# Optimization experiments

Measured on AMD Instinct MI355X. Metric: run time of the kernel, lower is better.

Reference implementation:

```python
import jax, jax.numpy as jnp
import numpy as np

V, D, L, H, T = 32000, 1024, 4, 16, 1024
DH = D // H
SCALE = DH ** -0.5
FF = 4 * D
R = 2  # n_rounds


def setup_inputs() -> dict:
    key = jax.random.key(0)
    ks = iter(jax.random.split(key, 32))
    s = 0.02
    nrm = lambda shape: jax.random.normal(next(ks), shape, dtype=jnp.float32) * s
    inp = {
        "x": jax.random.randint(next(ks), (2, T), 0, V),
        "embed": nrm((V, D)),
        "pos_embed": nrm((T, D)),
        "Wqkv": nrm((L, R, 3 * D, D)),
        "bqkv": jnp.zeros((L, R, 3 * D), jnp.float32),
        "Wo": nrm((L, D, D)),
        "bo": jnp.zeros((L, D), jnp.float32),
        "Wg": nrm((L, D, 2 * D)),
        "bg": jnp.zeros((L, D), jnp.float32),
        "ln1_g": jnp.ones((L, D), jnp.float32),
        "ln1_b": jnp.zeros((L, D), jnp.float32),
        "W1": nrm((L, FF, D)),
        "b1": jnp.zeros((L, FF), jnp.float32),
        "W2": nrm((L, D, FF)),
        "b2": jnp.zeros((L, D), jnp.float32),
        "ln2_g": jnp.ones((L, D), jnp.float32),
        "ln2_b": jnp.zeros((L, D), jnp.float32),
        "lnf_g": jnp.ones((D,), jnp.float32),
        "lnf_b": jnp.zeros((D,), jnp.float32),
    }
    return inp


def _ln(h, g, b, eps=1e-5):
    m = jnp.mean(h, axis=-1, keepdims=True)
    v = jnp.mean((h - m) ** 2, axis=-1, keepdims=True)
    return (h - m) * jax.lax.rsqrt(v + eps) * g + b


def _attend(h, W, b, mask):
    B, Tq, _ = h.shape
    qkv = (h @ W.T + b).reshape(B, Tq, 3, H, DH)
    q, k, v = qkv[:, :, 0], qkv[:, :, 1], qkv[:, :, 2]  # [B,T,H,DH]
    scores = jnp.einsum("bqhd,bkhd->bhqk", q, k) * SCALE
    scores = jnp.where(mask, scores, -jnp.inf)
    a = jax.nn.softmax(scores, axis=-1)
    return jnp.einsum("bhqk,bkhd->bqhd", a, v).reshape(B, Tq, D)


def reference(x, embed, pos_embed, Wqkv, bqkv, Wo, bo, Wg, bg,
              ln1_g, ln1_b, W1, b1, W2, b2, ln2_g, ln2_b, lnf_g, lnf_b):
    B, Tq = x.shape
    mask = jnp.tril(jnp.ones((Tq, Tq), dtype=bool))
    h = embed[x] + pos_embed[jnp.arange(Tq)]
    for l in range(L):
        n1 = _ln(h, ln1_g[l], ln1_b[l])
        pred = _attend(n1, Wqkv[l, 0], bqkv[l, 0], mask)
        cum = pred
        out = pred
        # boosted round 2: attend on residual, gate the correction
        corr = _attend(n1 - cum, Wqkv[l, 1], bqkv[l, 1], mask)
        gate = jax.nn.sigmoid(jnp.concatenate([cum, corr], axis=-1) @ Wg[l].T + bg[l])
        gated = gate * corr
        out = out + gated
        h = h + (out @ Wo[l].T + bo[l])
        n2 = _ln(h, ln2_g[l], ln2_b[l])
        ff = jax.nn.gelu(n2 @ W1[l].T + b1[l], approximate=False) @ W2[l].T + b2[l]
        h = h + ff
    return _ln(h, lnf_g, lnf_b) @ embed.T  # tied head, no bias
```

## Files before the change

kernel.cpp:

```cpp
#include <hip/hip_runtime.h>
#include <math.h>

#define D_  1024
#define T_  1024
#define B_  2
#define H_  16
#define DH_ 64
#define L_  4
#define FF_ 4096
#define V_  32000
#define M_  2048

typedef _Float16 f16;
typedef _Float16 f16x8 __attribute__((ext_vector_type(8)));
typedef _Float16 f16x4 __attribute__((ext_vector_type(4)));
typedef float    fx4  __attribute__((ext_vector_type(4)));

__global__ __launch_bounds__(256) void f2h_k(const float* __restrict__ in, f16* __restrict__ out) {
    const long i = ((long)blockIdx.x * 256 + threadIdx.x) * 4;
    const float4 v = *(const float4*)(in + i);
    f16x4 o = { (f16)v.x, (f16)v.y, (f16)v.z, (f16)v.w };
    *(f16x4*)(out + i) = o;
}

__global__ __launch_bounds__(256) void embed_k(const int* __restrict__ x, const float* __restrict__ emb,
                                               const float* __restrict__ pos, float* __restrict__ h) {
    const long m = blockIdx.x;
    const int  t = threadIdx.x;
    const long tok = x[m];
    const long pt  = m & (T_ - 1);
    const float4 e = ((const float4*)(emb + tok * D_))[t];
    const float4 p = ((const float4*)(pos + pt * D_))[t];
    ((float4*)(h + m * D_))[t] = make_float4(e.x + p.x, e.y + p.y, e.z + p.z, e.w + p.w);
}

__global__ __launch_bounds__(256) void ln_k(const float* __restrict__ x, const float* __restrict__ g,
                                            const float* __restrict__ b, float* __restrict__ of,
                                            f16* __restrict__ oh) {
    const long m = blockIdx.x;
    const int  t = threadIdx.x;
    const int  wave = t >> 6, lane = t & 63;
    __shared__ float red1[4], red2[4];
    const float4 v = ((const float4*)(x + m * D_))[t];
    float s = v.x + v.y + v.z + v.w;
#pragma unroll
    for (int off = 32; off; off >>= 1) s += __shfl_xor(s, off, 64);
    if (lane == 0) red1[wave] = s;
    __syncthreads();
    const float mean = (red1[0] + red1[1] + red1[2] + red1[3]) * (1.0f / 1024.0f);
    const float d0 = v.x - mean, d1 = v.y - mean, d2 = v.z - mean, d3 = v.w - mean;
    float s2 = d0 * d0 + d1 * d1 + d2 * d2 + d3 * d3;
#pragma unroll
    for (int off = 32; off; off >>= 1) s2 += __shfl_xor(s2, off, 64);
    if (lane == 0) red2[wave] = s2;
    __syncthreads();
    const float var  = (red2[0] + red2[1] + red2[2] + red2[3]) * (1.0f / 1024.0f);
    const float rstd = rsqrtf(var + 1e-5f);
    const float4 gv = ((const float4*)g)[t];
    const float4 bv = ((const float4*)b)[t];
    const float o0 = d0 * rstd * gv.x + bv.x;
    const float o1 = d1 * rstd * gv.y + bv.y;
    const float o2 = d2 * rstd * gv.z + bv.z;
    const float o3 = d3 * rstd * gv.w + bv.w;
    if (of) ((float4*)(of + m * D_))[t] = make_float4(o0, o1, o2, o3);
    if (oh) { f16x4 o = { (f16)o0, (f16)o1, (f16)o2, (f16)o3 }; *(f16x4*)(oh + m * D_ + t * 4) = o; }
}

__global__ __launch_bounds__(256) void sub_k(const float* __restrict__ a, const float* __restrict__ b,
                                             f16* __restrict__ o) {
    const long i = ((long)blockIdx.x * 256 + threadIdx.x) * 4;
    const float4 va = *(const float4*)(a + i);
    const float4 vb = *(const float4*)(b + i);
    f16x4 o4 = { (f16)(va.x - vb.x), (f16)(va.y - vb.y), (f16)(va.z - vb.z), (f16)(va.w - vb.w) };
    *(f16x4*)(o + i) = o4;
}

__global__ __launch_bounds__(256) void cat_k(const float* __restrict__ p, const float* __restrict__ c,
                                             f16* __restrict__ o) {
    const long i = ((long)blockIdx.x * 256 + threadIdx.x) * 4;
    const long m = i >> 11;
    const int  j = (int)(i & 2047);
    const float* src = (j < 1024) ? (p + m * 1024 + j) : (c + m * 1024 + (j - 1024));
    const float4 v = *(const float4*)src;
    f16x4 o4 = { (f16)v.x, (f16)v.y, (f16)v.z, (f16)v.w };
    *(f16x4*)(o + i) = o4;
}

__global__ __launch_bounds__(256) void gate_k(const float* __restrict__ p, const float* __restrict__ c,
                                              const float* __restrict__ gl, f16* __restrict__ o) {
    const long i = ((long)blockIdx.x * 256 + threadIdx.x) * 4;
    const float4 vp = *(const float4*)(p + i);
    const float4 vc = *(const float4*)(c + i);
    const float4 vg = *(const float4*)(gl + i);
    const float s0 = 1.0f / (1.0f + __expf(-vg.x));
    const float s1 = 1.0f / (1.0f + __expf(-vg.y));
    const float s2 = 1.0f / (1.0f + __expf(-vg.z));
    const float s3 = 1.0f / (1.0f + __expf(-vg.w));
    f16x4 o4 = { (f16)(vp.x + s0 * vc.x), (f16)(vp.y + s1 * vc.y),
                 (f16)(vp.z + s2 * vc.z), (f16)(vp.w + s3 * vc.w) };
    *(f16x4*)(o + i) = o4;
}

template<int BN>
__global__ __launch_bounds__(256)
void gemm_bt(const f16* __restrict__ A, const f16* __restrict__ Wt,
             const float* __restrict__ bias, const float* __restrict__ resid,
             float* __restrict__ Cf, f16* __restrict__ Ch,
             int N, int K, int gelu) {
    __shared__ __align__(16) f16 As[128 * 32];
    __shared__ __align__(16) f16 Bs[BN * 32];
    const int tid  = threadIdx.x;
    const int wave = tid >> 6;
    const int lane = tid & 63;

    const int nbm = gridDim.y;
    const int nbn = gridDim.x;
    int bi = blockIdx.y * nbn + blockIdx.x;
    const int nwg = nbm * nbn;
    if ((nwg & 7) == 0) bi = (bi & 7) * (nwg >> 3) + (bi >> 3);
    const long bm = bi % nbm;
    const long bn = bi / nbm;

    const int wm = (wave >> 1) * 64;
    const int wn = (wave & 1) * (BN / 2);
    constexpr int NJ = BN / 32;

    fx4 acc[4][NJ] = {};

    const int c0 = wave * 2;
    const int r0 = c0 * 16 + (lane >> 2);
    const int cc = (lane & 3) * 8;
    const f16* a0 = A + ((long)bm * 128 + r0) * K + cc;
    const f16* a1 = A + ((long)bm * 128 + r0 + 16) * K + cc;
    f16* sa0 = &As[c0 * 512];
    f16* sa1 = &As[(c0 + 1) * 512];

    const f16* b0;
    const f16* b1 = nullptr;
    f16* sb0;
    f16* sb1 = nullptr;
    if constexpr (BN == 128) {
        b0  = Wt + ((long)bn * 128 + r0) * K + cc;
        b1  = Wt + ((long)bn * 128 + r0 + 16) * K + cc;
        sb0 = &Bs[c0 * 512];
        sb1 = &Bs[(c0 + 1) * 512];
    } else {
        b0  = Wt + ((long)bn * 64 + wave * 16 + (lane >> 2)) * K + cc;
        sb0 = &Bs[wave * 512];
    }

    for (int k0 = 0; k0 < K; k0 += 32) {
        __builtin_amdgcn_global_load_lds((const __attribute__((address_space(1))) void*)(a0 + k0),
                                         (__attribute__((address_space(3))) void*)sa0, 16, 0, 0);
        __builtin_amdgcn_global_load_lds((const __attribute__((address_space(1))) void*)(a1 + k0),
                                         (__attribute__((address_space(3))) void*)sa1, 16, 0, 0);
        __builtin_amdgcn_global_load_lds((const __attribute__((address_space(1))) void*)(b0 + k0),
                                         (__attribute__((address_space(3))) void*)sb0, 16, 0, 0);
        if constexpr (BN == 128)
            __builtin_amdgcn_global_load_lds((const __attribute__((address_space(1))) void*)(b1 + k0),
                                             (__attribute__((address_space(3))) void*)sb1, 16, 0, 0);
        __syncthreads();
        const int koff = (lane >> 4) * 8;
        f16x8 af[4], bf[NJ];
#pragma unroll
        for (int i = 0; i < 4; ++i)
            af[i] = *(const f16x8*)&As[(wm + i * 16 + (lane & 15)) * 32 + koff];
#pragma unroll
        for (int j = 0; j < NJ; ++j)
            bf[j] = *(const f16x8*)&Bs[(wn + j * 16 + (lane & 15)) * 32 + koff];
#pragma unroll
        for (int i = 0; i < 4; ++i)
#pragma unroll
            for (int j = 0; j < NJ; ++j)
                acc[i][j] = __builtin_amdgcn_mfma_f32_16x16x32_f16(af[i], bf[j], acc[i][j], 0, 0, 0);
        __syncthreads();
    }

    const long gr_base = bm * 128 + wm + (lane >> 4) * 4;
    const long gc_base = bn * BN + wn + (lane & 15);
#pragma unroll
    for (int i = 0; i < 4; ++i) {
#pragma unroll
        for (int j = 0; j < NJ; ++j) {
            const long gc = gc_base + j * 16;
            const float bv = bias ? bias[gc] : 0.0f;
#pragma unroll
            for (int r = 0; r < 4; ++r) {
                const long gr = gr_base + i * 16 + r;
                float v = acc[i][j][r] + bv;
                if (gelu) v = 0.5f * v * (1.0f + erff(v * 0.70710678118654752f));
                else if (resid) v += resid[gr * (long)N + gc];
                if (Cf) Cf[gr * (long)N + gc] = v;
                if (Ch) Ch[gr * (long)N + gc] = (f16)v;
            }
        }
    }
}

__global__ __launch_bounds__(256) void fattn_k(const f16* __restrict__ qkv, float* __restrict__ out) {
    __shared__ __align__(16) f16 Ks[64 * 72];
    __shared__ __align__(16) f16 Vt[64 * 72];
    __shared__ __align__(16) f16 Pw[4][16 * 72];
    const int tid  = threadIdx.x;
    const int w    = tid >> 6;
    const int lane = tid & 63;
    const int b  = blockIdx.z, h = blockIdx.y;
    const int qt = (gridDim.x - 1) - blockIdx.x;
    const int q0w = qt * 64 + w * 16;
    const int g  = lane >> 4;
    const int lm = lane & 15;

    const long qrow = ((long)(b * T_ + q0w + lm)) * (3 * D_) + h * DH_;
    f16x8 af_q[2];
    af_q[0] = *(const f16x8*)(qkv + qrow + g * 8);
    af_q[1] = *(const f16x8*)(qkv + qrow + 32 + g * 8);

    float m_r[4], l_r[4];
    fx4 acc_o[4] = {};
#pragma unroll
    for (int r = 0; r < 4; ++r) { m_r[r] = -INFINITY; l_r[r] = 0.0f; }

    const int srow = tid >> 2;
    const int scol = (tid & 3) * 16;
    const long kbase = ((long)(b * T_)) * (3 * D_) + D_ + h * DH_ + scol;
    const long vbase = kbase + D_;

    const int nkb = qt + 1;
    for (int it = 0; it < nkb; ++it) {
        const int kb = it * 64;
        __syncthreads();
        {
            const f16* ksrc = qkv + kbase + (long)(kb + srow) * (3 * D_);
            f16x8 k0 = *(const f16x8*)(ksrc);
            f16x8 k1 = *(const f16x8*)(ksrc + 8);
            *(f16x8*)&Ks[srow * 72 + scol]     = k0;
            *(f16x8*)&Ks[srow * 72 + scol + 8] = k1;
            const f16* vsrc = qkv + vbase + (long)(kb + srow) * (3 * D_);
            f16x8 v0 = *(const f16x8*)(vsrc);
            f16x8 v1 = *(const f16x8*)(vsrc + 8);
#pragma unroll
            for (int i = 0; i < 8; ++i) {
                const int d = scol + i;
                Vt[d * 72 + (srow ^ (((d >> 2) & 7) << 3))] = v0[i];
            }
#pragma unroll
            for (int i = 0; i < 8; ++i) {
                const int d = scol + 8 + i;
                Vt[d * 72 + (srow ^ (((d >> 2) & 7) << 3))] = v1[i];
            }
        }
        __syncthreads();

        fx4 sc[4];
#pragma unroll
        for (int kt = 0; kt < 4; ++kt) {
            fx4 c = {};
#pragma unroll
            for (int kk = 0; kk < 2; ++kk) {
                f16x8 bf = *(const f16x8*)&Ks[(kt * 16 + lm) * 72 + kk * 32 + g * 8];
                c = __builtin_amdgcn_mfma_f32_16x16x32_f16(af_q[kk], bf, c, 0, 0, 0);
            }
            sc[kt] = c * 0.125f;
        }
        if (kb == qt * 64) {
#pragma unroll
            for (int kt = 0; kt < 4; ++kt) {
                const int key_g = kb + kt * 16 + lm;
#pragma unroll
                for (int r = 0; r < 4; ++r)
                    if (key_g > q0w + g * 4 + r) sc[kt][r] = -INFINITY;
            }
        }

        float mnew[4], pscale[4];
#pragma unroll
        for (int r = 0; r < 4; ++r) {
            float tm = fmaxf(fmaxf(sc[0][r], sc[1][r]), fmaxf(sc[2][r], sc[3][r]));
#pragma unroll
            for (int off = 8; off; off >>= 1) tm = fmaxf(tm, __shfl_xor(tm, off, 64));
            mnew[r]   = fmaxf(m_r[r], tm);
            pscale[r] = __expf(m_r[r] - mnew[r]);
        }
        float psum[4] = {};
#pragma unroll
        for (int kt = 0; kt < 4; ++kt) {
#pragma unroll
            for (int r = 0; r < 4; ++r) {
                const float p = __expf(sc[kt][r] - mnew[r]);
                sc[kt][r] = p;
                psum[r] += p;
            }
        }
#pragma unroll
        for (int r = 0; r < 4; ++r) {
#pragma unroll
            for (int off = 8; off; off >>= 1) psum[r] += __shfl_xor(psum[r], off, 64);
            l_r[r] = l_r[r] * pscale[r] + psum[r];
            m_r[r] = mnew[r];
        }
#pragma unroll
        for (int nt = 0; nt < 4; ++nt)
#pragma unroll
            for (int r = 0; r < 4; ++r) acc_o[nt][r] *= pscale[r];

        f16* P = Pw[w];
#pragma unroll
        for (int kt = 0; kt < 4; ++kt)
#pragma unroll
            for (int r = 0; r < 4; ++r)
                P[(g * 4 + r) * 72 + kt * 16 + lm] = (f16)sc[kt][r];

#pragma unroll
        for (int kc = 0; kc < 2; ++kc) {
            f16x8 ap = *(const f16x8*)&P[lm * 72 + kc * 32 + g * 8];
#pragma unroll
            for (int nt = 0; nt < 4; ++nt) {
                const int d = nt * 16 + lm;
                const int col = (kc * 32 + g * 8) ^ (((d >> 2) & 7) << 3);
                f16x8 bv = *(const f16x8*)&Vt[d * 72 + col];
                acc_o[nt] = __builtin_amdgcn_mfma_f32_16x16x32_f16(ap, bv, acc_o[nt], 0, 0, 0);
            }
        }
    }

    const long obase = ((long)(b * T_ + q0w + g * 4)) * D_ + h * DH_ + lm;
#pragma unroll
    for (int r = 0; r < 4; ++r) {
        const float inv = 1.0f / l_r[r];
#pragma unroll
        for (int nt = 0; nt < 4; ++nt)
            out[obase + (long)r * D_ + nt * 16] = acc_o[nt][r] * inv;
    }
}

extern "C" void kernel_launch(void* const* d_in, const int* in_sizes, int n_in,
                              void* d_out, int out_size, void* d_ws, size_t ws_size,
                              hipStream_t stream) {
    const int*   x    = (const int*)d_in[0];
    const float* emb  = (const float*)d_in[1];
    const float* pos  = (const float*)d_in[2];
    const float* Wqkv = (const float*)d_in[3];
    const float* bqkv = (const float*)d_in[4];
    const float* Wo   = (const float*)d_in[5];
    const float* bo   = (const float*)d_in[6];
    const float* Wg   = (const float*)d_in[7];
    const float* bg   = (const float*)d_in[8];
    const float* ln1g = (const float*)d_in[9];
    const float* ln1b = (const float*)d_in[10];
    const float* W1   = (const float*)d_in[11];
    const float* b1   = (const float*)d_in[12];
    const float* W2   = (const float*)d_in[13];
    const float* b2   = (const float*)d_in[14];
    const float* ln2g = (const float*)d_in[15];
    const float* ln2b = (const float*)d_in[16];
    const float* lnfg = (const float*)d_in[17];
    const float* lnfb = (const float*)d_in[18];
    float* out = (float*)d_out;

    char* ws = (char*)d_ws;
    size_t off = 0;
    auto alloc = [&](size_t bytes) -> void* {
        off = (off + 255) & ~(size_t)255;
        void* p = ws + off;
        off += bytes;
        return p;
    };
    float* h    = (float*)alloc((size_t)M_ * D_ * 4);
    float* n1f  = (float*)alloc((size_t)M_ * D_ * 4);
    float* pred = (float*)alloc((size_t)M_ * D_ * 4);
    float* corr = (float*)alloc((size_t)M_ * D_ * 4);
    float* glin = (float*)alloc((size_t)M_ * D_ * 4);
    f16* qkvh  = (f16*)alloc((size_t)M_ * 3 * D_ * 2);
    f16* ab    = (f16*)alloc((size_t)M_ * D_ * 2);
    f16* catb  = (f16*)alloc((size_t)M_ * 2 * D_ * 2);
    f16* ffh   = (f16*)alloc((size_t)M_ * FF_ * 2);
    f16* embh  = (f16*)alloc((size_t)V_ * D_ * 2);
    f16* wqkvh = (f16*)alloc((size_t)L_ * 2 * 3 * D_ * D_ * 2);
    f16* woh   = (f16*)alloc((size_t)L_ * D_ * D_ * 2);
    f16* wgh   = (f16*)alloc((size_t)L_ * D_ * 2 * D_ * 2);
    f16* w1h   = (f16*)alloc((size_t)L_ * FF_ * D_ * 2);
    f16* w2h   = (f16*)alloc((size_t)L_ * D_ * FF_ * 2);

    auto cvt = [&](const float* src, f16* dst, long n) {
        f2h_k<<<dim3((unsigned)(n / 1024)), dim3(256), 0, stream>>>(src, dst);
    };
    cvt(emb,  embh,  (long)V_ * D_);
    cvt(Wqkv, wqkvh, (long)L_ * 2 * 3 * D_ * D_);
    cvt(Wo,   woh,   (long)L_ * D_ * D_);
    cvt(Wg,   wgh,   (long)L_ * D_ * 2 * D_);
    cvt(W1,   w1h,   (long)L_ * FF_ * D_);
    cvt(W2,   w2h,   (long)L_ * D_ * FF_);

    embed_k<<<dim3(M_), dim3(256), 0, stream>>>(x, emb, pos, h);

    auto gemm = [&](const f16* A, const f16* Wt, const float* bias, const float* resid,
                    float* Cf, f16* Ch, int N, int K, int gelu) {
        if (N <= 1024)
            gemm_bt<64><<<dim3(N / 64, M_ / 128), dim3(256), 0, stream>>>(A, Wt, bias, resid, Cf, Ch, N, K, gelu);
        else
            gemm_bt<128><<<dim3(N / 128, M_ / 128), dim3(256), 0, stream>>>(A, Wt, bias, resid, Cf, Ch, N, K, gelu);
    };

    for (int l = 0; l < L_; ++l) {
        ln_k<<<dim3(M_), 256, 0, stream>>>(h, ln1g + l * D_, ln1b + l * D_, n1f, ab);
        gemm(ab, wqkvh + (size_t)(l * 2 + 0) * 3 * D_ * D_, bqkv + (l * 2 + 0) * 3 * D_,
             nullptr, nullptr, qkvh, 3 * D_, D_, 0);
        fattn_k<<<dim3(T_ / 64, H_, B_), 256, 0, stream>>>(qkvh, pred);
        sub_k<<<dim3(M_ * D_ / 1024), 256, 0, stream>>>(n1f, pred, ab);
        gemm(ab, wqkvh + (size_t)(l * 2 + 1) * 3 * D_ * D_, bqkv + (l * 2 + 1) * 3 * D_,
             nullptr, nullptr, qkvh, 3 * D_, D_, 0);
        fattn_k<<<dim3(T_ / 64, H_, B_), 256, 0, stream>>>(qkvh, corr);
        cat_k<<<dim3(M_ * 2 * D_ / 1024), 256, 0, stream>>>(pred, corr, catb);
        gemm(catb, wgh + (size_t)l * D_ * 2 * D_, bg + l * D_, nullptr, glin, nullptr, D_, 2 * D_, 0);
        gate_k<<<dim3(M_ * D_ / 1024), 256, 0, stream>>>(pred, corr, glin, ab);
        gemm(ab, woh + (size_t)l * D_ * D_, bo + l * D_, h, h, nullptr, D_, D_, 0);
        ln_k<<<dim3(M_), 256, 0, stream>>>(h, ln2g + l * D_, ln2b + l * D_, nullptr, ab);
        gemm(ab, w1h + (size_t)l * FF_ * D_, b1 + l * FF_, nullptr, nullptr, ffh, FF_, D_, 1);
        gemm(ffh, w2h + (size_t)l * D_ * FF_, b2 + l * D_, h, h, nullptr, D_, FF_, 0);
    }
    ln_k<<<dim3(M_), 256, 0, stream>>>(h, lnfg, lnfb, nullptr, ab);
    gemm(ab, embh, nullptr, nullptr, out, nullptr, V_, D_, 0);
}
```

Before: 2.339 ms.

## Triple-buffer GEMM LDS tiles with async global_load_lds prefetch

The shared GEMM kernel now uses a three-stage LDS ring buffer. It prefetches K-tiles two iterations ahead with global_load_lds and waits only for the current tile through explicit vmcnt counts, replacing the single-buffer load/sync/compute loop. The aim is to hide global memory latency behind MFMA work. In exchange it triples LDS use, which may reduce occupancy, and it depends on hand-tuned waitcnt values being exact for correctness.

```diff
diff --git a/kernel.cpp b/kernel.cpp
--- a/kernel.cpp
+++ b/kernel.cpp
@@ -107,8 +107,8 @@
              const float* __restrict__ bias, const float* __restrict__ resid,
              float* __restrict__ Cf, f16* __restrict__ Ch,
              int N, int K, int gelu) {
-    __shared__ __align__(16) f16 As[128 * 32];
-    __shared__ __align__(16) f16 Bs[BN * 32];
+    __shared__ __align__(16) f16 As[3][128 * 32];
+    __shared__ __align__(16) f16 Bs[3][BN * 32];
     const int tid  = threadIdx.x;
     const int wave = tid >> 6;
     const int lane = tid & 63;
@@ -132,48 +132,73 @@
     const int cc = (lane & 3) * 8;
     const f16* a0 = A + ((long)bm * 128 + r0) * K + cc;
     const f16* a1 = A + ((long)bm * 128 + r0 + 16) * K + cc;
-    f16* sa0 = &As[c0 * 512];
-    f16* sa1 = &As[(c0 + 1) * 512];
 
     const f16* b0;
     const f16* b1 = nullptr;
-    f16* sb0;
-    f16* sb1 = nullptr;
     if constexpr (BN == 128) {
-        b0  = Wt + ((long)bn * 128 + r0) * K + cc;
-        b1  = Wt + ((long)bn * 128 + r0 + 16) * K + cc;
-        sb0 = &Bs[c0 * 512];
-        sb1 = &Bs[(c0 + 1) * 512];
+        b0 = Wt + ((long)bn * 128 + r0) * K + cc;
+        b1 = Wt + ((long)bn * 128 + r0 + 16) * K + cc;
     } else {
-        b0  = Wt + ((long)bn * 64 + wave * 16 + (lane >> 2)) * K + cc;
-        sb0 = &Bs[wave * 512];
-    }
-
-    for (int k0 = 0; k0 < K; k0 += 32) {
+        b0 = Wt + ((long)bn * 64 + wave * 16 + (lane >> 2)) * K + cc;
+    }
+
+    const int NT = K >> 5;
+
+    auto STAGE = [&](int kt) {
+        const int k0 = kt * 32;
+        const int bf3 = kt % 3;
         __builtin_amdgcn_global_load_lds((const __attribute__((address_space(1))) void*)(a0 + k0),
-                                         (__attribute__((address_space(3))) void*)sa0, 16, 0, 0);
+                                         (__attribute__((address_space(3))) void*)&As[bf3][c0 * 512], 16, 0, 0);
         __builtin_amdgcn_global_load_lds((const __attribute__((address_space(1))) void*)(a1 + k0),
-                                         (__attribute__((address_space(3))) void*)sa1, 16, 0, 0);
-        __builtin_amdgcn_global_load_lds((const __attribute__((address_space(1))) void*)(b0 + k0),
-                                         (__attribute__((address_space(3))) void*)sb0, 16, 0, 0);
-        if constexpr (BN == 128)
+                                         (__attribute__((address_space(3))) void*)&As[bf3][(c0 + 1) * 512], 16, 0, 0);
+        if constexpr (BN == 128) {
+            __builtin_amdgcn_global_load_lds((const __attribute__((address_space(1))) void*)(b0 + k0),
+                                             (__attribute__((address_space(3))) void*)&Bs[bf3][c0 * 512], 16, 0, 0);
             __builtin_amdgcn_global_load_lds((const __attribute__((address_space(1))) void*)(b1 + k0),
-                                             (__attribute__((address_space(3))) void*)sb1, 16, 0, 0);
-        __syncthreads();
-        const int koff = (lane >> 4) * 8;
+                                             (__attribute__((address_space(3))) void*)&Bs[bf3][(c0 + 1) * 512], 16, 0, 0);
+        } else {
+            __builtin_amdgcn_global_load_lds((const __attribute__((address_space(1))) void*)(b0 + k0),
+                                             (__attribute__((address_space(3))) void*)&Bs[bf3][wave * 512], 16, 0, 0);
+        }
+    };
+
+    STAGE(0);
+    if (NT > 1) STAGE(1);
+
+    const int koff = (lane >> 4) * 8;
+    for (int t = 0; t < NT; ++t) {
+        if (t + 2 < NT) STAGE(t + 2);
+        const int rem = NT - 1 - t;
+        if constexpr (BN == 128) {
+            if (rem >= 2)      asm volatile("s_waitcnt vmcnt(8)" ::: "memory");
+            else if (rem == 1) asm volatile("s_waitcnt vmcnt(4)" ::: "memory");
+            else               asm volatile("s_waitcnt vmcnt(0)" ::: "memory");
+        } else {
+            if (rem >= 2)      asm volatile("s_waitcnt vmcnt(6)" ::: "memory");
+            else if (rem == 1) asm volatile("s_waitcnt vmcnt(3)" ::: "memory");
+            else               asm volatile("s_waitcnt vmcnt(0)" ::: "memory");
+        }
+        __builtin_amdgcn_s_barrier();
+        __builtin_amdgcn_sched_barrier(0);
+
+        const f16* as = As[t % 3];
+        const f16* bs = Bs[t % 3];
         f16x8 af[4], bf[NJ];
 #pragma unroll
         for (int i = 0; i < 4; ++i)
-            af[i] = *(const f16x8*)&As[(wm + i * 16 + (lane & 15)) * 32 + koff];
+            af[i] = *(const f16x8*)&as[(wm + i * 16 + (lane & 15)) * 32 + koff];
 #pragma unroll
         for (int j = 0; j < NJ; ++j)
-            bf[j] = *(const f16x8*)&Bs[(wn + j * 16 + (lane & 15)) * 32 + koff];
+            bf[j] = *(const f16x8*)&bs[(wn + j * 16 + (lane & 15)) * 32 + koff];
 #pragma unroll
         for (int i = 0; i < 4; ++i)
 #pragma unroll
             for (int j = 0; j < NJ; ++j)
                 acc[i][j] = __builtin_amdgcn_mfma_f32_16x16x32_f16(af[i], bf[j], acc[i][j], 0, 0, 0);
-        __syncthreads();
+
+        asm volatile("s_waitcnt lgkmcnt(0)" ::: "memory");
+        __builtin_amdgcn_sched_barrier(0);
+        __builtin_amdgcn_s_barrier();
     }
 
     const long gr_base = bm * 128 + wm + (lane >> 4) * 4;
```

Result: no change. 2.295 ms (-1.9%).
